# Performance work log

Hardware: AMD Instinct MI355X
Metric: run time of the kernel (lower is better)

Reference implementation:

```python
import jax, jax.numpy as jnp
import numpy as np

B, S, D, H = 4, 2048, 768, 8
HD = D // H
EPS = 1e-5
NEG = -1e9


def setup_inputs() -> dict:
    key = jax.random.key(0)
    ks = jax.random.split(key, 12)
    s = 1.0 / np.sqrt(D)
    inp = {
        "hidden_states": jax.random.normal(ks[0], (B, S, D), dtype=jnp.float32),
        "anchor_mask": jax.random.bernoulli(ks[1], 0.5, (B, S)),
        "ln_g": jnp.ones((D,), jnp.float32),
        "ln_b": jnp.zeros((D,), jnp.float32),
        "Wq": jax.random.uniform(ks[2], (D, D), jnp.float32, -s, s),
        "bq": jax.random.uniform(ks[3], (D,), jnp.float32, -s, s),
        "Wk": jax.random.uniform(ks[4], (D, D), jnp.float32, -s, s),
        "bk": jax.random.uniform(ks[5], (D,), jnp.float32, -s, s),
        "Wv": jax.random.uniform(ks[6], (D, D), jnp.float32, -s, s),
        "bv": jax.random.uniform(ks[7], (D,), jnp.float32, -s, s),
        "Wo": jax.random.uniform(ks[8], (D, D), jnp.float32, -s, s),
        "bo": jax.random.uniform(ks[9], (D,), jnp.float32, -s, s),
    }
    return inp


def reference(hidden_states, anchor_mask, ln_g, ln_b, Wq, bq, Wk, bk, Wv, bv, Wo, bo):
    # LayerNorm (per-token, so applying to all tokens == applying to gathered anchors)
    mu = jnp.mean(hidden_states, axis=-1, keepdims=True)
    var = jnp.mean(jnp.square(hidden_states - mu), axis=-1, keepdims=True)
    x = (hidden_states - mu) * jax.lax.rsqrt(var + EPS) * ln_g + ln_b

    # QKV projections: torch Linear is x @ W.T + b
    q = (jnp.einsum('bsd,ed->bse', x, Wq) + bq).reshape(B, S, H, HD)
    k = (jnp.einsum('bsd,ed->bse', x, Wk) + bk).reshape(B, S, H, HD)
    v = (jnp.einsum('bsd,ed->bse', x, Wv) + bv).reshape(B, S, H, HD)

    scale = 1.0 / np.sqrt(HD)
    scores = jnp.einsum('bqhd,bkhd->bhqk', q, k) * scale
    # keys restricted to anchor positions (equivalent to the gather)
    key_mask = anchor_mask[:, None, None, :]  # (B,1,1,S)
    scores = jnp.where(key_mask, scores, NEG)
    attn = jax.nn.softmax(scores, axis=-1)  # dropout is identity in eval

    out = jnp.einsum('bhqk,bkhd->bqhd', attn, v).reshape(B, S, D)
    out = jnp.einsum('bsd,ed->bse', out, Wo) + bo
    # scatter back: zeros at non-anchor positions
    return out * anchor_mask[:, :, None].astype(out.dtype)
```

## Files before the change

kernel.cpp:

```cpp
#include <hip/hip_runtime.h>
#include <math.h>

#define S_LEN 2048
#define D_DIM 768
#define NH 8
#define HD 96
#define NTOK 8192

typedef short bf16x8 __attribute__((ext_vector_type(8)));
typedef float f32x4 __attribute__((ext_vector_type(4)));

__device__ __forceinline__ f32x4 mfma16(bf16x8 a, bf16x8 b, f32x4 c) {
    return __builtin_amdgcn_mfma_f32_16x16x32_bf16(a, b, c, 0, 0, 0);
}

__device__ __forceinline__ unsigned short f2bf(float f) {
    unsigned int u = __float_as_uint(f);
    u += 0x7fffu + ((u >> 16) & 1u);
    return (unsigned short)(u >> 16);
}

__device__ __forceinline__ void gl_lds16(const unsigned short* g, unsigned short* l) {
    __builtin_amdgcn_global_load_lds(
        (const __attribute__((address_space(1))) unsigned int*)g,
        (__attribute__((address_space(3))) unsigned int*)l, 16, 0, 0);
}

#define TILE_SHORTS 6144
#define BH_SHORTS   196608

__global__ __launch_bounds__(256) void prep_kernel(
    const unsigned char* __restrict__ mb, int* __restrict__ idx, int* __restrict__ cnt,
    const float* __restrict__ Wq, const float* __restrict__ Wk,
    const float* __restrict__ Wv, const float* __restrict__ Wo,
    unsigned short* __restrict__ W4b, float* __restrict__ out)
{
    const int bi = blockIdx.x;
    const int t  = threadIdx.x;

    if (bi < 4) {
        __shared__ int red[4];
        __shared__ int warp_tot[4];
        const int b = bi;
        int s = 0;
        for (int i = t; i < NTOK; i += 256) s += (int)mb[i];
        for (int off = 32; off > 0; off >>= 1) s += __shfl_down(s, off, 64);
        if ((t & 63) == 0) red[t >> 6] = s;
        __syncthreads();
        const int total = red[0] + red[1] + red[2] + red[3];
        const int mode = (total > 20000) ? 2 : ((total > 2500) ? 1 : 0);
        const int*   mi = (const int*)mb;
        const float* mf = (const float*)mb;
        const int p0 = t * 8;
        int av = 0, c = 0;
        #pragma unroll
        for (int j = 0; j < 8; ++j) {
            const int g = b * S_LEN + p0 + j;
            bool a;
            if (mode == 2)      a = (mf[g] != 0.0f);
            else if (mode == 1) a = (mb[g] != 0);
            else                a = (mi[g] != 0);
            if (a) { av |= (1 << j); ++c; }
        }
        const int lane = t & 63, w = t >> 6;
        int v = c;
        #pragma unroll
        for (int off = 1; off < 64; off <<= 1) {
            const int u = __shfl_up(v, off, 64);
            if (lane >= off) v += u;
        }
        if (lane == 63) warp_tot[w] = v;
        __syncthreads();
        int wbase = 0;
        for (int i = 0; i < w; ++i) wbase += warp_tot[i];
        int o = wbase + v - c;
        #pragma unroll
        for (int j = 0; j < 8; ++j)
            if (av & (1 << j)) idx[b * S_LEN + (o++)] = p0 + j;
        if (t == 255) cnt[b] = wbase + v;
    } else if (bi < 1156) {
        const int i = bi - 4;
        const int w = i / 288, blk = i % 288;
        const float* src = (w == 0) ? Wq : (w == 1) ? Wk : (w == 2) ? Wv : Wo;
        const int base = (blk * 256 + t) * 8;
        const float4 a = *(const float4*)&src[base];
        const float4 c = *(const float4*)&src[base + 4];
        uint4 u;
        u.x = (unsigned int)f2bf(a.x) | ((unsigned int)f2bf(a.y) << 16);
        u.y = (unsigned int)f2bf(a.z) | ((unsigned int)f2bf(a.w) << 16);
        u.z = (unsigned int)f2bf(c.x) | ((unsigned int)f2bf(c.y) << 16);
        u.w = (unsigned int)f2bf(c.z) | ((unsigned int)f2bf(c.w) << 16);
        *(uint4*)&W4b[(size_t)w * 589824 + base] = u;
    } else {
        const size_t i4 = (size_t)(bi - 1156) * 256 + t;
        float4 z; z.x = z.y = z.z = z.w = 0.0f;
        *(float4*)&out[i4 * 4] = z;
    }
}

__global__ __launch_bounds__(256) void ln_gather_kernel(
    const float* __restrict__ H, const float* __restrict__ g,
    const float* __restrict__ bta, const int* __restrict__ idx,
    const int* __restrict__ cnt, unsigned short* __restrict__ X)
{
    __shared__ float rs[4], rss[4];
    const int slot = blockIdx.x;
    const int b = slot >> 11, r = slot & (S_LEN - 1);
    if (r >= cnt[b]) return;
    const int p = idx[slot];
    const float* hr = H + (size_t)(b * S_LEN + p) * D_DIM;
    unsigned short* xr = X + (size_t)slot * D_DIM;
    const int t = threadIdx.x;
    const float v0 = hr[t], v1 = hr[t + 256], v2 = hr[t + 512];
    float s  = v0 + v1 + v2;
    float ss = v0*v0 + v1*v1 + v2*v2;
    for (int off = 32; off > 0; off >>= 1) {
        s  += __shfl_down(s,  off, 64);
        ss += __shfl_down(ss, off, 64);
    }
    if ((t & 63) == 0) { rs[t >> 6] = s; rss[t >> 6] = ss; }
    __syncthreads();
    const float sum = rs[0] + rs[1] + rs[2] + rs[3];
    const float sq  = rss[0] + rss[1] + rss[2] + rss[3];
    const float mu  = sum * (1.0f / D_DIM);
    const float var = sq * (1.0f / D_DIM) - mu * mu;
    const float rstd = rsqrtf(var + 1e-5f);
    xr[t]       = f2bf((v0 - mu) * rstd * g[t]       + bta[t]);
    xr[t + 256] = f2bf((v1 - mu) * rstd * g[t + 256] + bta[t + 256]);
    xr[t + 512] = f2bf((v2 - mu) * rstd * g[t + 512] + bta[t + 512]);
}

__global__ __launch_bounds__(256) void gemm_bf16(
    const unsigned short* __restrict__ A,
    const unsigned short* __restrict__ W4,
    const float* __restrict__ b0, const float* __restrict__ b1,
    const float* __restrict__ b2,
    const int* __restrict__ cnt, const int* __restrict__ idx,
    unsigned short* __restrict__ Qo, unsigned short* __restrict__ Kp,
    unsigned short* __restrict__ Vp, float* __restrict__ Fo,
    int oproj)
{
    const int z = blockIdx.z;
    const int m0 = blockIdx.y * 128;
    const int b  = m0 >> 11;
    const int rbase = m0 & (S_LEN - 1);
    const int nc = cnt[b];
    if (rbase >= nc) return;
    const int n0 = blockIdx.x * 128;
    const unsigned short* W = W4 + (size_t)z * 589824;
    const float* bias = (z == 0) ? b0 : (z == 1 ? b1 : b2);

    __shared__ unsigned short Al[128 * 32];
    __shared__ unsigned short Bl[128 * 32];

    const int t = threadIdx.x;
    const int srow = t >> 2, sg = t & 3;
    const int ra0 = b * S_LEN + min(rbase + srow,      nc - 1);
    const int ra1 = b * S_LEN + min(rbase + srow + 64, nc - 1);
    const unsigned short* gA0 = A + (size_t)ra0 * 768 + sg * 8;
    const unsigned short* gA1 = A + (size_t)ra1 * 768 + sg * 8;
    const unsigned short* gB0 = W + (size_t)(n0 + srow)      * 768 + sg * 8;
    const unsigned short* gB1 = W + (size_t)(n0 + srow + 64) * 768 + sg * 8;
    unsigned short* lA = Al + t * 8;
    unsigned short* lB = Bl + t * 8;

    const int w = t >> 6, lane = t & 63;
    const int l15 = lane & 15, quad = lane >> 4;
    const int mh = (w & 1) * 64, nh2 = (w >> 1) * 64;

    f32x4 acc[4][4] = {};

    int aoff[4], boff[4];
    #pragma unroll
    for (int i = 0; i < 4; ++i) {
        aoff[i] = (mh  + i * 16 + l15) * 32 + quad * 8;
        boff[i] = (nh2 + i * 16 + l15) * 32 + quad * 8;
    }

    for (int k0 = 0; k0 < 768; k0 += 32) {
        __syncthreads();
        gl_lds16(gA0 + k0, lA);
        gl_lds16(gA1 + k0, lA + 2048);
        gl_lds16(gB0 + k0, lB);
        gl_lds16(gB1 + k0, lB + 2048);
        __syncthreads();
        bf16x8 af[4], bfr[4];
        #pragma unroll
        for (int i = 0; i < 4; ++i) af[i]  = *(const bf16x8*)(Al + aoff[i]);
        #pragma unroll
        for (int i = 0; i < 4; ++i) bfr[i] = *(const bf16x8*)(Bl + boff[i]);
        #pragma unroll
        for (int ms = 0; ms < 4; ++ms)
            #pragma unroll
            for (int ns = 0; ns < 4; ++ns)
                acc[ms][ns] = mfma16(af[ms], bfr[ns], acc[ms][ns]);
    }

    if (!oproj) {
        if (z == 0) {
            #pragma unroll
            for (int ns = 0; ns < 4; ++ns) {
                const int n = n0 + nh2 + ns * 16 + l15;
                const float bv = bias[n];
                #pragma unroll
                for (int ms = 0; ms < 4; ++ms) {
                    const int ml = mh + ms * 16 + quad * 4;
                    #pragma unroll
                    for (int r = 0; r < 4; ++r) {
                        const int slot = b * S_LEN + rbase + ml + r;
                        Qo[(size_t)slot * 768 + n] = f2bf(acc[ms][ns][r] + bv);
                    }
                }
            }
        } else if (z == 1) {
            #pragma unroll
            for (int ns = 0; ns < 4; ++ns) {
                const int n = n0 + nh2 + ns * 16 + l15;
                const int h = n / 96, d = n - h * 96;
                const float bv = bias[n];
                unsigned short* base = Kp + (size_t)(b * 8 + h) * BH_SHORTS;
                const int dseg = d >> 3, dlo = d & 7;
                #pragma unroll
                for (int ms = 0; ms < 4; ++ms) {
                    const int ml = mh + ms * 16 + quad * 4;
                    #pragma unroll
                    for (int r = 0; r < 4; ++r) {
                        const int tok = rbase + ml + r;
                        const int kt = tok >> 6, tk = tok & 63;
                        const int g16 = tk >> 4, lr = tk & 15;
                        base[(size_t)kt * TILE_SHORTS +
                             (g16 * 192 + dseg * 16 + lr) * 8 + dlo] =
                            f2bf(acc[ms][ns][r] + bv);
                    }
                }
            }
        } else {
            #pragma unroll
            for (int ns = 0; ns < 4; ++ns) {
                const int n = n0 + nh2 + ns * 16 + l15;
                const int h = n / 96, d = n - h * 96;
                const float bv = bias[n];
                unsigned short* base = Vp + (size_t)(b * 8 + h) * BH_SHORTS;
                const int dg = d >> 4, l16 = d & 15;
                #pragma unroll
                for (int ms = 0; ms < 4; ++ms) {
                    const int ml = mh + ms * 16 + quad * 4;
                    const int k = rbase + ml;
                    const int kt = k >> 6, tk = k & 63;
                    const int kseg = tk >> 3, klo = tk & 7;
                    const unsigned short h0 = f2bf(acc[ms][ns][0] + bv);
                    const unsigned short h1 = f2bf(acc[ms][ns][1] + bv);
                    const unsigned short h2 = f2bf(acc[ms][ns][2] + bv);
                    const unsigned short h3 = f2bf(acc[ms][ns][3] + bv);
                    uint2 u;
                    u.x = (unsigned int)h0 | ((unsigned int)h1 << 16);
                    u.y = (unsigned int)h2 | ((unsigned int)h3 << 16);
                    *(uint2*)&base[(size_t)kt * TILE_SHORTS +
                                   (dg * 128 + kseg * 16 + l16) * 8 + klo] = u;
                }
            }
        }
    } else {
        #pragma unroll
        for (int ns = 0; ns < 4; ++ns) {
            const int n = n0 + nh2 + ns * 16 + l15;
            const float bv = bias[n];
            #pragma unroll
            for (int ms = 0; ms < 4; ++ms) {
                const int ml = mh + ms * 16 + quad * 4;
                #pragma unroll
                for (int r = 0; r < 4; ++r) {
                    const int rloc = rbase + ml + r;
                    if (rloc < nc) {
                        const int orow = b * S_LEN + idx[b * S_LEN + rloc];
                        Fo[(size_t)orow * 768 + n] = acc[ms][ns][r] + bv;
                    }
                }
            }
        }
    }
}

__global__ __launch_bounds__(256) void attn_mfma(
    const unsigned short* __restrict__ Q,
    const unsigned short* __restrict__ Kp,
    const unsigned short* __restrict__ Vp,
    const int* __restrict__ cnt,
    unsigned short* __restrict__ O)
{
    const int q0 = blockIdx.x * 64;
    const int h  = blockIdx.y;
    const int b  = blockIdx.z;
    const int nk = cnt[b];
    if (q0 >= nk) return;

    __shared__ unsigned short SB[6144 + 6144 + 4 * 1152];
    unsigned short* Kl = SB;
    unsigned short* Vl = SB + 6144;

    const int t = threadIdx.x, w = t >> 6, lane = t & 63;
    const int l15 = lane & 15, quad = lane >> 4;
    const int qw = q0 + w * 16;
    const int bS = b * S_LEN;
    const float CE = 0.14724459f;

    const unsigned short* Kbh = Kp + (size_t)(b * 8 + h) * BH_SHORTS + t * 8;
    const unsigned short* Vbh = Vp + (size_t)(b * 8 + h) * BH_SHORTS + t * 8;

    const unsigned short* qrow = Q + (size_t)(bS + qw + l15) * 768 + h * 96 + quad * 8;
    bf16x8 qf[3];
    qf[0] = *(const bf16x8*)(qrow);
    qf[1] = *(const bf16x8*)(qrow + 32);
    qf[2] = *(const bf16x8*)(qrow + 64);

    unsigned short* Pw = SB + 12288 + w * 1152;
    float lsum = 0.0f;
    f32x4 oacc[6] = {};

    const int kts = (nk + 63) >> 6;
    for (int kt = 0; kt < kts; ++kt) {
        const size_t tb = (size_t)kt * TILE_SHORTS;
        __syncthreads();
        #pragma unroll
        for (int r = 0; r < 3; ++r) {
            gl_lds16(Kbh + tb + r * 2048, Kl + r * 2048 + t * 8);
            gl_lds16(Vbh + tb + r * 2048, Vl + r * 2048 + t * 8);
        }
        __syncthreads();
        const int k0 = kt * 64;

        const int lim = nk - k0;
        #pragma unroll
        for (int s = 0; s < 4; ++s) {
            f32x4 sa = {};
            #pragma unroll
            for (int ks = 0; ks < 3; ++ks) {
                const bf16x8 kf = *(const bf16x8*)(Kl + (s * 192 + (quad + ks * 4) * 16 + l15) * 8);
                sa = mfma16(kf, qf[ks], sa);
            }
            unsigned short pk[4];
            #pragma unroll
            for (int r = 0; r < 4; ++r) {
                float p = exp2f(sa[r] * CE);
                p = (s * 16 + quad * 4 + r < lim) ? p : 0.0f;
                lsum += p;
                pk[r] = f2bf(p);
            }
            uint2 u;
            u.x = (unsigned int)pk[0] | ((unsigned int)pk[1] << 16);
            u.y = (unsigned int)pk[2] | ((unsigned int)pk[3] << 16);
            *(uint2*)&Pw[l15 * 72 + s * 16 + quad * 4] = u;
        }

        const bf16x8 pb0 = *(const bf16x8*)(Pw + l15 * 72 + quad * 8);
        const bf16x8 pb1 = *(const bf16x8*)(Pw + l15 * 72 + 32 + quad * 8);

        #pragma unroll
        for (int dt = 0; dt < 6; ++dt) {
            const bf16x8 v0f = *(const bf16x8*)(Vl + (dt * 128 + quad * 16 + l15) * 8);
            const bf16x8 v1f = *(const bf16x8*)(Vl + (dt * 128 + (quad + 4) * 16 + l15) * 8);
            oacc[dt] = mfma16(v0f, pb0, oacc[dt]);
            oacc[dt] = mfma16(v1f, pb1, oacc[dt]);
        }
    }

    lsum += __shfl_xor(lsum, 16);
    lsum += __shfl_xor(lsum, 32);

    const int qi = qw + l15;
    if (qi < nk) {
        const float rl = 1.0f / lsum;
        unsigned short* og = O + (size_t)(bS + qi) * 768 + h * 96;
        #pragma unroll
        for (int dt = 0; dt < 6; ++dt) {
            const unsigned short o0 = f2bf(oacc[dt][0] * rl);
            const unsigned short o1 = f2bf(oacc[dt][1] * rl);
            const unsigned short o2 = f2bf(oacc[dt][2] * rl);
            const unsigned short o3 = f2bf(oacc[dt][3] * rl);
            uint2 u;
            u.x = (unsigned int)o0 | ((unsigned int)o1 << 16);
            u.y = (unsigned int)o2 | ((unsigned int)o3 << 16);
            *(uint2*)&og[dt * 16 + quad * 4] = u;
        }
    }
}

extern "C" void kernel_launch(void* const* d_in, const int* in_sizes, int n_in,
                              void* d_out, int out_size, void* d_ws, size_t ws_size,
                              hipStream_t stream)
{
    const float* hs  = (const float*)d_in[0];
    const unsigned char* am = (const unsigned char*)d_in[1];
    const float* lng = (const float*)d_in[2];
    const float* lnb = (const float*)d_in[3];
    const float* Wq  = (const float*)d_in[4];
    const float* bq  = (const float*)d_in[5];
    const float* Wk  = (const float*)d_in[6];
    const float* bk  = (const float*)d_in[7];
    const float* Wv  = (const float*)d_in[8];
    const float* bv  = (const float*)d_in[9];
    const float* Wo  = (const float*)d_in[10];
    const float* bo  = (const float*)d_in[11];

    char* ws = (char*)d_ws;
    const size_t BUF = (size_t)NTOK * 768 * 2;
    int* idx = (int*)ws;
    int* cnt = (int*)(ws + 32768);
    unsigned short* xb  = (unsigned short*)(ws + 65536);
    unsigned short* Qb  = (unsigned short*)(ws + 65536 + BUF);
    unsigned short* Kpb = (unsigned short*)(ws + 65536 + 2 * BUF);
    unsigned short* Vpb = (unsigned short*)(ws + 65536 + 3 * BUF);
    unsigned short* W4b = (unsigned short*)(ws + 65536 + 4 * BUF);
    unsigned short* Ob  = xb;
    float* out = (float*)d_out;

    prep_kernel<<<dim3(2692), dim3(256), 0, stream>>>(
        am, idx, cnt, Wq, Wk, Wv, Wo, W4b, out);

    ln_gather_kernel<<<dim3(NTOK), dim3(256), 0, stream>>>(hs, lng, lnb, idx, cnt, xb);

    gemm_bf16<<<dim3(6, 64, 3), dim3(256), 0, stream>>>(
        xb, W4b, bq, bk, bv, cnt, idx, Qb, Kpb, Vpb, nullptr, 0);

    attn_mfma<<<dim3(32, NH, 4), dim3(256), 0, stream>>>(Qb, Kpb, Vpb, cnt, Ob);

    gemm_bf16<<<dim3(6, 64, 1), dim3(256), 0, stream>>>(
        Ob, W4b + (size_t)3 * 589824, bo, bo, bo, cnt, idx,
        nullptr, nullptr, nullptr, out, 1);
}
```

Measured before the change: 223.1 us.

## Double-buffer K/V tiles in attention and move key masking into projection

The attention kernel now double-buffers K/V tiles in LDS, prefetching the next tile while computing the current one, which removes one barrier per iteration. The per-element key mask is gone: the projection writes zeros for padded K/V rows, and the padded keys' exp(0)=1 contributions are subtracted from the row sum afterwards. The kernel also raises wave priority around the MFMA sections and flattens the grid so consecutive blocks cover different batch-head pairs. LDS use doubles, which may lower occupancy.

Measured after the change: 217.6 us. 1.03x faster.

```diff
diff --git a/kernel.cpp b/kernel.cpp
--- a/kernel.cpp
+++ b/kernel.cpp
@@ -230,7 +230,8 @@
                         const int g16 = tk >> 4, lr = tk & 15;
                         base[(size_t)kt * TILE_SHORTS +
                              (g16 * 192 + dseg * 16 + lr) * 8 + dlo] =
-                            f2bf(acc[ms][ns][r] + bv);
+                            (tok < nc) ? f2bf(acc[ms][ns][r] + bv)
+                                       : (unsigned short)0;
                     }
                 }
             }
@@ -248,10 +249,14 @@
                     const int k = rbase + ml;
                     const int kt = k >> 6, tk = k & 63;
                     const int kseg = tk >> 3, klo = tk & 7;
-                    const unsigned short h0 = f2bf(acc[ms][ns][0] + bv);
-                    const unsigned short h1 = f2bf(acc[ms][ns][1] + bv);
-                    const unsigned short h2 = f2bf(acc[ms][ns][2] + bv);
-                    const unsigned short h3 = f2bf(acc[ms][ns][3] + bv);
+                    const unsigned short h0 =
+                        (k + 0 < nc) ? f2bf(acc[ms][ns][0] + bv) : (unsigned short)0;
+                    const unsigned short h1 =
+                        (k + 1 < nc) ? f2bf(acc[ms][ns][1] + bv) : (unsigned short)0;
+                    const unsigned short h2 =
+                        (k + 2 < nc) ? f2bf(acc[ms][ns][2] + bv) : (unsigned short)0;
+                    const unsigned short h3 =
+                        (k + 3 < nc) ? f2bf(acc[ms][ns][3] + bv) : (unsigned short)0;
                     uint2 u;
                     u.x = (unsigned int)h0 | ((unsigned int)h1 << 16);
                     u.y = (unsigned int)h2 | ((unsigned int)h3 << 16);
@@ -288,15 +293,13 @@
     const int* __restrict__ cnt,
     unsigned short* __restrict__ O)
 {
-    const int q0 = blockIdx.x * 64;
-    const int h  = blockIdx.y;
-    const int b  = blockIdx.z;
+    const int bh = blockIdx.x & 31;
+    const int b  = bh >> 3, h = bh & 7;
+    const int q0 = (blockIdx.x >> 5) * 64;
     const int nk = cnt[b];
     if (q0 >= nk) return;
 
-    __shared__ unsigned short SB[6144 + 6144 + 4 * 1152];
-    unsigned short* Kl = SB;
-    unsigned short* Vl = SB + 6144;
+    __shared__ unsigned short SB[2 * 12288 + 4 * 1152];
 
     const int t = threadIdx.x, w = t >> 6, lane = t & 63;
     const int l15 = lane & 15, quad = lane >> 4;
@@ -304,8 +307,9 @@
     const int bS = b * S_LEN;
     const float CE = 0.14724459f;
 
-    const unsigned short* Kbh = Kp + (size_t)(b * 8 + h) * BH_SHORTS + t * 8;
-    const unsigned short* Vbh = Vp + (size_t)(b * 8 + h) * BH_SHORTS + t * 8;
+    const int t8 = t * 8;
+    const unsigned short* Kst = Kp + (size_t)(b * 8 + h) * BH_SHORTS + t8;
+    const unsigned short* Vst = Vp + (size_t)(b * 8 + h) * BH_SHORTS + t8;
 
     const unsigned short* qrow = Q + (size_t)(bS + qw + l15) * 768 + h * 96 + quad * 8;
     bf16x8 qf[3];
@@ -313,36 +317,50 @@
     qf[1] = *(const bf16x8*)(qrow + 32);
     qf[2] = *(const bf16x8*)(qrow + 64);
 
-    unsigned short* Pw = SB + 12288 + w * 1152;
+    unsigned short* Pw   = SB + 24576 + w * 1152;
+    unsigned short* bufA = SB;
+    unsigned short* bufB = SB + 12288;
+
     float lsum = 0.0f;
     f32x4 oacc[6] = {};
 
     const int kts = (nk + 63) >> 6;
+
+    #pragma unroll
+    for (int r = 0; r < 3; ++r) {
+        gl_lds16(Kst + r * 2048, bufA + r * 2048 + t8);
+        gl_lds16(Vst + r * 2048, bufA + 6144 + r * 2048 + t8);
+    }
+    Kst += TILE_SHORTS; Vst += TILE_SHORTS;
+    __syncthreads();
+
     for (int kt = 0; kt < kts; ++kt) {
-        const size_t tb = (size_t)kt * TILE_SHORTS;
-        __syncthreads();
-        #pragma unroll
-        for (int r = 0; r < 3; ++r) {
-            gl_lds16(Kbh + tb + r * 2048, Kl + r * 2048 + t * 8);
-            gl_lds16(Vbh + tb + r * 2048, Vl + r * 2048 + t * 8);
-        }
-        __syncthreads();
-        const int k0 = kt * 64;
-
-        const int lim = nk - k0;
+        if (kt + 1 < kts) {
+            #pragma unroll
+            for (int r = 0; r < 3; ++r) {
+                gl_lds16(Kst + r * 2048, bufB + r * 2048 + t8);
+                gl_lds16(Vst + r * 2048, bufB + 6144 + r * 2048 + t8);
+            }
+            Kst += TILE_SHORTS; Vst += TILE_SHORTS;
+        }
+
+        const unsigned short* Kl = bufA;
+        const unsigned short* Vl = bufA + 6144;
+
         #pragma unroll
         for (int s = 0; s < 4; ++s) {
             f32x4 sa = {};
+            __builtin_amdgcn_s_setprio(1);
             #pragma unroll
             for (int ks = 0; ks < 3; ++ks) {
                 const bf16x8 kf = *(const bf16x8*)(Kl + (s * 192 + (quad + ks * 4) * 16 + l15) * 8);
                 sa = mfma16(kf, qf[ks], sa);
             }
+            __builtin_amdgcn_s_setprio(0);
             unsigned short pk[4];
             #pragma unroll
             for (int r = 0; r < 4; ++r) {
-                float p = exp2f(sa[r] * CE);
-                p = (s * 16 + quad * 4 + r < lim) ? p : 0.0f;
+                const float p = exp2f(sa[r] * CE);
                 lsum += p;
                 pk[r] = f2bf(p);
             }
@@ -355,6 +373,7 @@
         const bf16x8 pb0 = *(const bf16x8*)(Pw + l15 * 72 + quad * 8);
         const bf16x8 pb1 = *(const bf16x8*)(Pw + l15 * 72 + 32 + quad * 8);
 
+        __builtin_amdgcn_s_setprio(1);
         #pragma unroll
         for (int dt = 0; dt < 6; ++dt) {
             const bf16x8 v0f = *(const bf16x8*)(Vl + (dt * 128 + quad * 16 + l15) * 8);
@@ -362,10 +381,15 @@
             oacc[dt] = mfma16(v0f, pb0, oacc[dt]);
             oacc[dt] = mfma16(v1f, pb1, oacc[dt]);
         }
+        __builtin_amdgcn_s_setprio(0);
+
+        __syncthreads();
+        unsigned short* tmp = bufA; bufA = bufB; bufB = tmp;
     }
 
     lsum += __shfl_xor(lsum, 16);
     lsum += __shfl_xor(lsum, 32);
+    lsum -= (float)((kts << 6) - nk);
 
     const int qi = qw + l15;
     if (qi < nk) {
@@ -422,7 +446,7 @@
     gemm_bf16<<<dim3(6, 64, 3), dim3(256), 0, stream>>>(
         xb, W4b, bq, bk, bv, cnt, idx, Qb, Kpb, Vpb, nullptr, 0);
 
-    attn_mfma<<<dim3(32, NH, 4), dim3(256), 0, stream>>>(Qb, Kpb, Vpb, cnt, Ob);
+    attn_mfma<<<dim3(1024), dim3(256), 0, stream>>>(Qb, Kpb, Vpb, cnt, Ob);
 
     gemm_bf16<<<dim3(6, 64, 1), dim3(256), 0, stream>>>(
         Ob, W4b + (size_t)3 * 589824, bo, bo, bo, cnt, idx,
```
